# Kernel tuning notes

Measured on AMD Instinct MI355X. Metric: run time of the kernel, lower is better.

Reference implementation:

```python
import jax, jax.numpy as jnp
import numpy as np

N_NODES = 10000
N_EDGES = 320000
DIM = 256
NUM_HEADS = 8
HEAD_DIM = DIM // NUM_HEADS


def setup_inputs() -> dict:
    key = jax.random.key(0)
    ks = jax.random.split(key, 8)
    s = 1.0 / np.sqrt(DIM)
    x = jax.random.normal(ks[0], (N_NODES, DIM), dtype=jnp.float32)
    src = jax.random.randint(ks[1], (N_EDGES,), 0, N_NODES, dtype=jnp.int32)
    dst = jax.random.randint(ks[2], (N_EDGES,), 0, N_NODES, dtype=jnp.int32)
    Wq = jax.random.normal(ks[3], (DIM, DIM), dtype=jnp.float32) * s
    Wk = jax.random.normal(ks[4], (DIM, DIM), dtype=jnp.float32) * s
    Wv = jax.random.normal(ks[5], (DIM, DIM), dtype=jnp.float32) * s
    Wo = jax.random.normal(ks[6], (DIM, DIM), dtype=jnp.float32) * s
    z = jnp.zeros((DIM,), dtype=jnp.float32)
    return {"x": x, "src": src, "dst": dst,
            "Wq": Wq, "bq": z, "Wk": Wk, "bk": z,
            "Wv": Wv, "bv": z, "Wo": Wo, "bo": z}


def reference(x, src, dst, Wq, bq, Wk, bk, Wv, bv, Wo, bo):
    N = x.shape[0]
    # nn.Linear: y = x @ W.T + b
    q = (x @ Wq.T + bq).reshape(N, NUM_HEADS, HEAD_DIM)
    k = (x @ Wk.T + bk).reshape(N, NUM_HEADS, HEAD_DIM)
    v = (x @ Wv.T + bv).reshape(N, NUM_HEADS, HEAD_DIM)
    # u_dot_v: dot(q[src], k[dst]) per head -> [E, H]
    score = jnp.einsum('ehd,ehd->eh', q[src], k[dst]) / np.sqrt(HEAD_DIM).astype(np.float32)
    # Faithful to source: F.softmax(dim=1) on [E, H, 1] -> softmax over HEADS axis
    attn = jax.nn.softmax(score, axis=1)  # [E, H]
    # u_mul_e then sum-reduce onto destination nodes
    m = v[src] * attn[:, :, None]  # [E, H, HEAD_DIM]
    h = jax.ops.segment_sum(m, dst, num_segments=N).reshape(N, DIM)
    out = h @ Wo.T + bo
    # dropout p=0.0 -> identity
    return out
```

## Files before the change

### kernel.cpp

```cpp
#include <hip/hip_runtime.h>
#include <stdint.h>

#define N_NODES 10000
#define N_EDGES 320000
#define DIM 256
#define NRANGE 4
#define RANGE_DIV 2500
#define PAD_SLOTS 32

typedef _Float16 half8 __attribute__((ext_vector_type(8)));
typedef _Float16 half2t __attribute__((ext_vector_type(2)));
typedef float floatx4 __attribute__((ext_vector_type(4)));

#define QK_SCALE 0.17677669529663687f

typedef __attribute__((address_space(3))) uint32_t lds_u32;
typedef __attribute__((address_space(1))) const uint32_t glob_u32;
__device__ __forceinline__ void load16_lds(const _Float16* g, _Float16* l) {
  __builtin_amdgcn_global_load_lds((glob_u32*)g, (lds_u32*)l, 16, 0, 0);
}

__device__ __forceinline__ half8 cvt8s(const float4 a, const float4 b, float sc) {
  half8 o;
  o[0] = (_Float16)(a.x * sc); o[1] = (_Float16)(a.y * sc);
  o[2] = (_Float16)(a.z * sc); o[3] = (_Float16)(a.w * sc);
  o[4] = (_Float16)(b.x * sc); o[5] = (_Float16)(b.y * sc);
  o[6] = (_Float16)(b.z * sc); o[7] = (_Float16)(b.w * sc);
  return o;
}

__global__ void __launch_bounds__(256) prep_k(
    const float* __restrict__ x, const float* __restrict__ Wq,
    const float* __restrict__ Wk, const float* __restrict__ Wv,
    const float* __restrict__ Wo, const int* __restrict__ src,
    const int* __restrict__ dst,
    _Float16* __restrict__ xh, _Float16* __restrict__ Wcat,
    _Float16* __restrict__ Woh, int* __restrict__ cnt4,
    int* __restrict__ slist4) {
  int b = blockIdx.x;
  int t = threadIdx.x;
  if (b < 1250) {
    int i = b * 256 + t;
    const float4* p = (const float4*)x;
    ((half8*)xh)[i] = cvt8s(p[2 * i], p[2 * i + 1], 1.0f);
  } else if (b < 1378) {
    int bb = b - 1250;
    int w = bb >> 5;
    int i = (bb & 31) * 256 + t;
    const float* in = (w == 0) ? Wq : (w == 1) ? Wv : (w == 2) ? Wk : Wo;
    _Float16* out = (w < 3) ? (Wcat + (size_t)w * 65536) : Woh;
    float sc = (w == 0) ? QK_SCALE : 1.0f;
    const float4* p = (const float4*)in;
    ((half8*)out)[i] = cvt8s(p[2 * i], p[2 * i + 1], sc);
  } else {
    int e = (b - 1378) * 256 + t;
    int s = src[e];
    int r = s / RANGE_DIV;
    int cell = dst[e] * NRANGE + r;
    int pos = atomicAdd(&cnt4[cell], 1);
    if (pos < PAD_SLOTS) slist4[cell * PAD_SLOTS + pos] = s;
  }
}

template <int MODE>
__global__ void __launch_bounds__(256) gemm_tiled(
    const _Float16* __restrict__ A, const _Float16* __restrict__ B,
    const float* __restrict__ b0, const float* __restrict__ b1,
    const float* __restrict__ b2,
    _Float16* __restrict__ qv, _Float16* __restrict__ kh,
    float* __restrict__ outf, int M) {
  __shared__ _Float16 As[16384];
  __shared__ _Float16 Bs[16384];
  int t = threadIdx.x;
  int lane = t & 63;
  int wid = t >> 6;
  int l16 = lane & 15;
  int quad = lane >> 4;
  int wm = wid >> 1, wn = wid & 1;
  int m0 = blockIdx.x * 128;
  int n0 = blockIdx.y * 128;

  floatx4 acc[4][4];
#pragma unroll
  for (int i = 0; i < 4; ++i)
#pragma unroll
    for (int j = 0; j < 4; ++j) acc[i][j] = (floatx4){0.f, 0.f, 0.f, 0.f};

  auto stage = [&](int ks, int buf) {
#pragma unroll
    for (int i = 0; i < 4; ++i) {
      int idx = i * 4 + wid;
      int c = idx >> 1;
      int h = idx & 1;
      int r = h * 64 + lane;
      int ar = m0 + r;
      if (ar >= M) ar = M - 1;
      load16_lds(A + (size_t)ar * 256 + ks * 64 + c * 8,
                 &As[buf * 8192 + (c * 128 + h * 64) * 8]);
      load16_lds(B + (size_t)(n0 + r) * 256 + ks * 64 + c * 8,
                 &Bs[buf * 8192 + (c * 128 + h * 64) * 8]);
    }
  };

  stage(0, 0);
  __syncthreads();

  for (int ks = 0; ks < 4; ++ks) {
    int bsel = ks & 1;
    if (ks < 3) stage(ks + 1, 1 - bsel);
#pragma unroll
    for (int kk = 0; kk < 2; ++kk) {
      int j = kk * 4 + quad;
      half8 af[4], bf[4];
#pragma unroll
      for (int i = 0; i < 4; ++i) {
        af[i] = *(const half8*)&As[bsel * 8192 + (j * 128 + wm * 64 + i * 16 + l16) * 8];
        bf[i] = *(const half8*)&Bs[bsel * 8192 + (j * 128 + wn * 64 + i * 16 + l16) * 8];
      }
#pragma unroll
      for (int mi = 0; mi < 4; ++mi)
#pragma unroll
        for (int ni = 0; ni < 4; ++ni)
          acc[mi][ni] =
              __builtin_amdgcn_mfma_f32_16x16x32_f16(af[mi], bf[ni], acc[mi][ni], 0, 0, 0);
    }
    __syncthreads();
  }

#pragma unroll
  for (int mi = 0; mi < 4; ++mi) {
#pragma unroll
    for (int ni = 0; ni < 4; ++ni) {
      int col = n0 + wn * 64 + ni * 16 + l16;
      float bias;
      if (MODE == 0) {
        bias = (col < 256) ? b0[col] * QK_SCALE
                           : (col < 512) ? b1[col - 256] : b2[col - 512];
      } else {
        bias = b0[col];
      }
#pragma unroll
      for (int r = 0; r < 4; ++r) {
        int row = m0 + wm * 64 + mi * 16 + quad * 4 + r;
        if (row < M) {
          float val = acc[mi][ni][r] + bias;
          if (MODE == 0) {
            if (col < 512)
              qv[(size_t)row * 512 + col] = (_Float16)val;
            else
              kh[(size_t)row * 256 + (col - 512)] = (_Float16)val;
          } else {
            outf[(size_t)row * 256 + col] = val;
          }
        }
      }
    }
  }
}

__global__ void __launch_bounds__(256, 4) aggregate_k(
    const _Float16* __restrict__ qv, const _Float16* __restrict__ kh,
    const int* __restrict__ slist4, const int* __restrict__ cnt4,
    _Float16* __restrict__ hh) {
  int lane = threadIdx.x & 63;
  int n = blockIdx.x * 4 + (threadIdx.x >> 6);
  if (n >= N_NODES) return;
  int h = lane & 7;
  int g = lane >> 3;

  int4 cv = ((const int4*)cnt4)[n];
  int d0 = min(cv.x, PAD_SLOTS), d1 = min(cv.y, PAD_SLOTS);
  int d2 = min(cv.z, PAD_SLOTS), d3 = min(cv.w, PAD_SLOTS);
  int o1 = d0, o2 = o1 + d1, o3 = o2 + d2;
  int T = o3 + d3;
  const int* nb = slist4 + (size_t)n * (NRANGE * PAD_SLOTS);

  int sidA = 0, sidB = 0;
  {
    int i0 = lane;
    int r0 = (i0 >= o1) + (i0 >= o2) + (i0 >= o3);
    int b0r = (r0 == 0) ? 0 : (r0 == 1) ? o1 : (r0 == 2) ? o2 : o3;
    if (i0 < T) sidA = nb[r0 * PAD_SLOTS + (i0 - b0r)];
    if (T > 64) {
      int i1 = lane + 64;
      int r1 = (i1 >= o1) + (i1 >= o2) + (i1 >= o3);
      int b1r = (r1 == 0) ? 0 : (r1 == 1) ? o1 : (r1 == 2) ? o2 : o3;
      if (i1 < T) sidB = nb[r1 * PAD_SLOTS + (i1 - b1r)];
    }
  }

  half8 kc[4];
  const half8* krow = (const half8*)(kh + (size_t)n * DIM + h * 32);
#pragma unroll
  for (int i = 0; i < 4; ++i) kc[i] = krow[i];
  const half2t* k2 = (const half2t*)kc;

  half2t acc[16];
#pragma unroll
  for (int i = 0; i < 16; ++i) acc[i] = (half2t){(_Float16)0.f, (_Float16)0.f};

  int iters = (T + 7) >> 3;
  if (iters > 0) {
    int s0 = __shfl(sidA, g);
    const half8* rr = (const half8*)(qv + (size_t)s0 * 512 + h * 32);
    half8 qc[4];
#pragma unroll
    for (int i = 0; i < 4; ++i) qc[i] = rr[i];
    bool valid = g < T;

#pragma unroll 1
    for (int jj = 0; jj < iters; ++jj) {
      half8 vc[4];
#pragma unroll
      for (int i = 0; i < 4; ++i) vc[i] = rr[32 + i];
      half8 nq[4];
      bool nvalid = false;
      const half8* nrr = rr;
      if (jj + 1 < iters) {
        int nidx = (jj + 1) * 8 + g;
        int ns = (jj + 1 < 8) ? __shfl(sidA, nidx) : __shfl(sidB, nidx - 64);
        nrr = (const half8*)(qv + (size_t)ns * 512 + h * 32);
#pragma unroll
        for (int i = 0; i < 4; ++i) nq[i] = nrr[i];
        nvalid = nidx < T;
      }
      const half2t* q2 = (const half2t*)qc;
      float pa = 0.f, pb = 0.f, pc = 0.f, pd = 0.f;
#pragma unroll
      for (int i = 0; i < 4; ++i) {
#if __has_builtin(__builtin_amdgcn_fdot2)
        pa = __builtin_amdgcn_fdot2(q2[i], k2[i], pa, false);
        pb = __builtin_amdgcn_fdot2(q2[4 + i], k2[4 + i], pb, false);
        pc = __builtin_amdgcn_fdot2(q2[8 + i], k2[8 + i], pc, false);
        pd = __builtin_amdgcn_fdot2(q2[12 + i], k2[12 + i], pd, false);
#else
        pa += (float)q2[i][0] * (float)k2[i][0] + (float)q2[i][1] * (float)k2[i][1];
        pb += (float)q2[4 + i][0] * (float)k2[4 + i][0] + (float)q2[4 + i][1] * (float)k2[4 + i][1];
        pc += (float)q2[8 + i][0] * (float)k2[8 + i][0] + (float)q2[8 + i][1] * (float)k2[8 + i][1];
        pd += (float)q2[12 + i][0] * (float)k2[12 + i][0] + (float)q2[12 + i][1] * (float)k2[12 + i][1];
#endif
      }
      float p = (pa + pb) + (pc + pd);
      float ex = __expf(p);
      float ssum = ex;
      ssum += __shfl_xor(ssum, 1);
      ssum += __shfl_xor(ssum, 2);
      ssum += __shfl_xor(ssum, 4);
      float a = valid ? (ex * __frcp_rn(ssum)) : 0.f;
      _Float16 ah = (_Float16)a;
      half2t ah2 = (half2t){ah, ah};
      const half2t* v2 = (const half2t*)vc;
#pragma unroll
      for (int i = 0; i < 16; ++i) acc[i] += v2[i] * ah2;
#pragma unroll
      for (int i = 0; i < 4; ++i) qc[i] = nq[i];
      rr = nrr;
      valid = nvalid;
    }
  }

#pragma unroll
  for (int i = 0; i < 16; ++i) {
    union { half2t h2; int v; } u;
    u.h2 = acc[i]; u.v = __shfl_xor(u.v, 8);  acc[i] += u.h2;
    u.h2 = acc[i]; u.v = __shfl_xor(u.v, 16); acc[i] += u.h2;
    u.h2 = acc[i]; u.v = __shfl_xor(u.v, 32); acc[i] += u.h2;
  }
  if (g == 0) {
    half8* hrow = (half8*)(hh + (size_t)n * DIM + h * 32);
    const half8* a8 = (const half8*)acc;
#pragma unroll
    for (int i = 0; i < 4; ++i) hrow[i] = a8[i];
  }
}

extern "C" void kernel_launch(void* const* d_in, const int* in_sizes, int n_in,
                              void* d_out, int out_size, void* d_ws, size_t ws_size,
                              hipStream_t stream) {
  const float* x = (const float*)d_in[0];
  const int* src = (const int*)d_in[1];
  const int* dst = (const int*)d_in[2];
  const float* Wq = (const float*)d_in[3];
  const float* bq = (const float*)d_in[4];
  const float* Wk = (const float*)d_in[5];
  const float* bk = (const float*)d_in[6];
  const float* Wv = (const float*)d_in[7];
  const float* bv = (const float*)d_in[8];
  const float* Wo = (const float*)d_in[9];
  const float* bo = (const float*)d_in[10];

  char* p = (char*)d_ws;
  const size_t SZ_NODE_H = (size_t)N_NODES * DIM * sizeof(_Float16);
  _Float16* xh = (_Float16*)p; p += SZ_NODE_H;
  _Float16* qvv = (_Float16*)p; p += 2 * SZ_NODE_H;
  _Float16* kh = (_Float16*)p; p += SZ_NODE_H;
  _Float16* hh = (_Float16*)p; p += SZ_NODE_H;
  _Float16* Wcat = (_Float16*)p; p += (size_t)768 * 256 * sizeof(_Float16);
  _Float16* Woh = (_Float16*)p; p += (size_t)256 * 256 * sizeof(_Float16);
  int* cnt4 = (int*)p; p += (size_t)N_NODES * NRANGE * sizeof(int);
  int* slist4 = (int*)p; p += (size_t)N_NODES * NRANGE * PAD_SLOTS * sizeof(int);

  hipMemsetAsync(cnt4, 0, (size_t)N_NODES * NRANGE * sizeof(int), stream);

  prep_k<<<2628, 256, 0, stream>>>(x, Wq, Wk, Wv, Wo, src, dst, xh, Wcat, Woh,
                                   cnt4, slist4);

  gemm_tiled<0><<<dim3(79, 6), 256, 0, stream>>>(xh, Wcat, bq, bv, bk, qvv, kh,
                                                 nullptr, N_NODES);

  aggregate_k<<<2500, 256, 0, stream>>>(qvv, kh, slist4, cnt4, hh);

  gemm_tiled<1><<<dim3(79, 2), 256, 0, stream>>>(hh, Woh, bo, nullptr, nullptr,
                                                 nullptr, nullptr, (float*)d_out,
                                                 N_NODES);
}
```

Before: 171.2 us.

## Overlap edge bucketing with QKV GEMM and fold counter zeroing into prep

The separate memset of the per-node counters is replaced by zeroing done inside the prep kernel. The edge-scatter step, which buckets source ids per destination and range with atomics, moves out of prep and into extra blocks of the QKV GEMM launch. This lets the atomic scatter run alongside the GEMM tiles and removes one memset call. The GEMM kernel is split into two specialised non-template kernels. The scatter blocks now compete with GEMM blocks for CUs, and each scatter block processes 582 edges in a strided loop.

```diff
diff --git a/kernel.cpp b/kernel.cpp
--- a/kernel.cpp
+++ b/kernel.cpp
@@ -32,11 +32,9 @@
 __global__ void __launch_bounds__(256) prep_k(
     const float* __restrict__ x, const float* __restrict__ Wq,
     const float* __restrict__ Wk, const float* __restrict__ Wv,
-    const float* __restrict__ Wo, const int* __restrict__ src,
-    const int* __restrict__ dst,
+    const float* __restrict__ Wo,
     _Float16* __restrict__ xh, _Float16* __restrict__ Wcat,
-    _Float16* __restrict__ Woh, int* __restrict__ cnt4,
-    int* __restrict__ slist4) {
+    _Float16* __restrict__ Woh, int* __restrict__ cnt4) {
   int b = blockIdx.x;
   int t = threadIdx.x;
   if (b < 1250) {
@@ -53,22 +51,122 @@
     const float4* p = (const float4*)in;
     ((half8*)out)[i] = cvt8s(p[2 * i], p[2 * i + 1], sc);
   } else {
-    int e = (b - 1378) * 256 + t;
-    int s = src[e];
-    int r = s / RANGE_DIV;
-    int cell = dst[e] * NRANGE + r;
-    int pos = atomicAdd(&cnt4[cell], 1);
-    if (pos < PAD_SLOTS) slist4[cell * PAD_SLOTS + pos] = s;
-  }
-}
-
-template <int MODE>
-__global__ void __launch_bounds__(256) gemm_tiled(
+    int idx = (b - 1378) * 256 + t;
+#pragma unroll
+    for (int k = 0; k < 4; ++k) {
+      int j = idx + k * 2560;
+      if (j < 10000) ((int4*)cnt4)[j] = (int4){0, 0, 0, 0};
+    }
+  }
+}
+
+__global__ void __launch_bounds__(256) gemm0_scatter_k(
     const _Float16* __restrict__ A, const _Float16* __restrict__ B,
     const float* __restrict__ b0, const float* __restrict__ b1,
     const float* __restrict__ b2,
     _Float16* __restrict__ qv, _Float16* __restrict__ kh,
-    float* __restrict__ outf, int M) {
+    const int* __restrict__ src, const int* __restrict__ dst,
+    int* __restrict__ cnt4, int* __restrict__ slist4) {
+  __shared__ _Float16 As[16384];
+  __shared__ _Float16 Bs[16384];
+  int u = blockIdx.x;
+  int t = threadIdx.x;
+
+  if (u >= 474) {
+    int e0 = (u - 474) * 582;
+    int e1 = e0 + 582;
+    if (e1 > N_EDGES) e1 = N_EDGES;
+    for (int e = e0 + t; e < e1; e += 256) {
+      int s = src[e];
+      int r = s / RANGE_DIV;
+      int cell = dst[e] * NRANGE + r;
+      int pos = atomicAdd(&cnt4[cell], 1);
+      if (pos < PAD_SLOTS) slist4[cell * PAD_SLOTS + pos] = s;
+    }
+    return;
+  }
+
+  int bx = u % 79, by = u / 79;
+  int lane = t & 63;
+  int wid = t >> 6;
+  int l16 = lane & 15;
+  int quad = lane >> 4;
+  int wm = wid >> 1, wn = wid & 1;
+  int m0 = bx * 128;
+  int n0 = by * 128;
+
+  floatx4 acc[4][4];
+#pragma unroll
+  for (int i = 0; i < 4; ++i)
+#pragma unroll
+    for (int j = 0; j < 4; ++j) acc[i][j] = (floatx4){0.f, 0.f, 0.f, 0.f};
+
+  auto stage = [&](int ks, int buf) {
+#pragma unroll
+    for (int i = 0; i < 4; ++i) {
+      int idx = i * 4 + wid;
+      int c = idx >> 1;
+      int h = idx & 1;
+      int r = h * 64 + lane;
+      int ar = m0 + r;
+      if (ar >= N_NODES) ar = N_NODES - 1;
+      load16_lds(A + (size_t)ar * 256 + ks * 64 + c * 8,
+                 &As[buf * 8192 + (c * 128 + h * 64) * 8]);
+      load16_lds(B + (size_t)(n0 + r) * 256 + ks * 64 + c * 8,
+                 &Bs[buf * 8192 + (c * 128 + h * 64) * 8]);
+    }
+  };
+
+  stage(0, 0);
+  __syncthreads();
+
+  for (int ks = 0; ks < 4; ++ks) {
+    int bsel = ks & 1;
+    if (ks < 3) stage(ks + 1, 1 - bsel);
+#pragma unroll
+    for (int kk = 0; kk < 2; ++kk) {
+      int j = kk * 4 + quad;
+      half8 af[4], bf[4];
+#pragma unroll
+      for (int i = 0; i < 4; ++i) {
+        af[i] = *(const half8*)&As[bsel * 8192 + (j * 128 + wm * 64 + i * 16 + l16) * 8];
+        bf[i] = *(const half8*)&Bs[bsel * 8192 + (j * 128 + wn * 64 + i * 16 + l16) * 8];
+      }
+#pragma unroll
+      for (int mi = 0; mi < 4; ++mi)
+#pragma unroll
+        for (int ni = 0; ni < 4; ++ni)
+          acc[mi][ni] =
+              __builtin_amdgcn_mfma_f32_16x16x32_f16(af[mi], bf[ni], acc[mi][ni], 0, 0, 0);
+    }
+    __syncthreads();
+  }
+
+#pragma unroll
+  for (int mi = 0; mi < 4; ++mi) {
+#pragma unroll
+    for (int ni = 0; ni < 4; ++ni) {
+      int col = n0 + wn * 64 + ni * 16 + l16;
+      float bias = (col < 256) ? b0[col] * QK_SCALE
+                               : (col < 512) ? b1[col - 256] : b2[col - 512];
+#pragma unroll
+      for (int r = 0; r < 4; ++r) {
+        int row = m0 + wm * 64 + mi * 16 + quad * 4 + r;
+        if (row < N_NODES) {
+          float val = acc[mi][ni][r] + bias;
+          if (col < 512)
+            qv[(size_t)row * 512 + col] = (_Float16)val;
+          else
+            kh[(size_t)row * 256 + (col - 512)] = (_Float16)val;
+        }
+      }
+    }
+  }
+}
+
+__global__ void __launch_bounds__(256) gemm1_k(
+    const _Float16* __restrict__ A, const _Float16* __restrict__ B,
+    const float* __restrict__ b0, float* __restrict__ outf) {
   __shared__ _Float16 As[16384];
   __shared__ _Float16 Bs[16384];
   int t = threadIdx.x;
@@ -94,7 +192,7 @@
       int h = idx & 1;
       int r = h * 64 + lane;
       int ar = m0 + r;
-      if (ar >= M) ar = M - 1;
+      if (ar >= N_NODES) ar = N_NODES - 1;
       load16_lds(A + (size_t)ar * 256 + ks * 64 + c * 8,
                  &As[buf * 8192 + (c * 128 + h * 64) * 8]);
       load16_lds(B + (size_t)(n0 + r) * 256 + ks * 64 + c * 8,
@@ -132,27 +230,12 @@
 #pragma unroll
     for (int ni = 0; ni < 4; ++ni) {
       int col = n0 + wn * 64 + ni * 16 + l16;
-      float bias;
-      if (MODE == 0) {
-        bias = (col < 256) ? b0[col] * QK_SCALE
-                           : (col < 512) ? b1[col - 256] : b2[col - 512];
-      } else {
-        bias = b0[col];
-      }
+      float bias = b0[col];
 #pragma unroll
       for (int r = 0; r < 4; ++r) {
         int row = m0 + wm * 64 + mi * 16 + quad * 4 + r;
-        if (row < M) {
-          float val = acc[mi][ni][r] + bias;
-          if (MODE == 0) {
-            if (col < 512)
-              qv[(size_t)row * 512 + col] = (_Float16)val;
-            else
-              kh[(size_t)row * 256 + (col - 512)] = (_Float16)val;
-          } else {
-            outf[(size_t)row * 256 + col] = val;
-          }
-        }
+        if (row < N_NODES)
+          outf[(size_t)row * 256 + col] = acc[mi][ni][r] + bias;
       }
     }
   }
@@ -300,17 +383,12 @@
   int* cnt4 = (int*)p; p += (size_t)N_NODES * NRANGE * sizeof(int);
   int* slist4 = (int*)p; p += (size_t)N_NODES * NRANGE * PAD_SLOTS * sizeof(int);
 
-  hipMemsetAsync(cnt4, 0, (size_t)N_NODES * NRANGE * sizeof(int), stream);
-
-  prep_k<<<2628, 256, 0, stream>>>(x, Wq, Wk, Wv, Wo, src, dst, xh, Wcat, Woh,
-                                   cnt4, slist4);
-
-  gemm_tiled<0><<<dim3(79, 6), 256, 0, stream>>>(xh, Wcat, bq, bv, bk, qvv, kh,
-                                                 nullptr, N_NODES);
+  prep_k<<<1388, 256, 0, stream>>>(x, Wq, Wk, Wv, Wo, xh, Wcat, Woh, cnt4);
+
+  gemm0_scatter_k<<<1024, 256, 0, stream>>>(xh, Wcat, bq, bv, bk, qvv, kh,
+                                            src, dst, cnt4, slist4);
 
   aggregate_k<<<2500, 256, 0, stream>>>(qvv, kh, slist4, cnt4, hh);
 
-  gemm_tiled<1><<<dim3(79, 2), 256, 0, stream>>>(hh, Woh, bo, nullptr, nullptr,
-                                                 nullptr, nullptr, (float*)d_out,
-                                                 N_NODES);
-}
+  gemm1_k<<<dim3(79, 2), 256, 0, stream>>>(hh, Woh, bo, (float*)d_out);
+}
```

Measured after the change: 165.8 us. 3.2% less time.

## Overlap edge scatter with QKV GEMM and halve GEMM K-tile LDS

Applied to the files above, without the earlier changes.

The edge bucketing scatter moves out of the prep kernel and into extra blocks of the QKV GEMM launch, so the atomics run alongside the matrix multiply. The counter memset is replaced by zeroing inside prep_k. The GEMM K-step shrinks from 64 to 32, which halves shared memory per block (allowing more resident blocks) but doubles the loop iterations and barriers. The cost is contention between the two kinds of blocks and more synchronisation per tile.

```diff
diff --git a/kernel.cpp b/kernel.cpp
--- a/kernel.cpp
+++ b/kernel.cpp
@@ -32,11 +32,9 @@
 __global__ void __launch_bounds__(256) prep_k(
     const float* __restrict__ x, const float* __restrict__ Wq,
     const float* __restrict__ Wk, const float* __restrict__ Wv,
-    const float* __restrict__ Wo, const int* __restrict__ src,
-    const int* __restrict__ dst,
+    const float* __restrict__ Wo,
     _Float16* __restrict__ xh, _Float16* __restrict__ Wcat,
-    _Float16* __restrict__ Woh, int* __restrict__ cnt4,
-    int* __restrict__ slist4) {
+    _Float16* __restrict__ Woh, int* __restrict__ cnt4) {
   int b = blockIdx.x;
   int t = threadIdx.x;
   if (b < 1250) {
@@ -53,32 +51,25 @@
     const float4* p = (const float4*)in;
     ((half8*)out)[i] = cvt8s(p[2 * i], p[2 * i + 1], sc);
   } else {
-    int e = (b - 1378) * 256 + t;
-    int s = src[e];
-    int r = s / RANGE_DIV;
-    int cell = dst[e] * NRANGE + r;
-    int pos = atomicAdd(&cnt4[cell], 1);
-    if (pos < PAD_SLOTS) slist4[cell * PAD_SLOTS + pos] = s;
-  }
-}
-
-template <int MODE>
-__global__ void __launch_bounds__(256) gemm_tiled(
+    int idx = (b - 1378) * 256 + t;
+#pragma unroll
+    for (int k = 0; k < 4; ++k) {
+      int j = idx + k * 2560;
+      if (j < 10000) ((int4*)cnt4)[j] = (int4){0, 0, 0, 0};
+    }
+  }
+}
+
+template <typename STORE>
+__device__ __forceinline__ void gemm_tile32(
+    _Float16* As, _Float16* Bs,
     const _Float16* __restrict__ A, const _Float16* __restrict__ B,
-    const float* __restrict__ b0, const float* __restrict__ b1,
-    const float* __restrict__ b2,
-    _Float16* __restrict__ qv, _Float16* __restrict__ kh,
-    float* __restrict__ outf, int M) {
-  __shared__ _Float16 As[16384];
-  __shared__ _Float16 Bs[16384];
-  int t = threadIdx.x;
+    int m0, int n0, int t, STORE&& store_fn) {
   int lane = t & 63;
   int wid = t >> 6;
   int l16 = lane & 15;
   int quad = lane >> 4;
   int wm = wid >> 1, wn = wid & 1;
-  int m0 = blockIdx.x * 128;
-  int n0 = blockIdx.y * 128;
 
   floatx4 acc[4][4];
 #pragma unroll
@@ -88,42 +79,38 @@
 
   auto stage = [&](int ks, int buf) {
 #pragma unroll
-    for (int i = 0; i < 4; ++i) {
+    for (int i = 0; i < 2; ++i) {
       int idx = i * 4 + wid;
       int c = idx >> 1;
-      int h = idx & 1;
-      int r = h * 64 + lane;
+      int hh2 = idx & 1;
+      int r = hh2 * 64 + lane;
       int ar = m0 + r;
-      if (ar >= M) ar = M - 1;
-      load16_lds(A + (size_t)ar * 256 + ks * 64 + c * 8,
-                 &As[buf * 8192 + (c * 128 + h * 64) * 8]);
-      load16_lds(B + (size_t)(n0 + r) * 256 + ks * 64 + c * 8,
-                 &Bs[buf * 8192 + (c * 128 + h * 64) * 8]);
+      if (ar >= N_NODES) ar = N_NODES - 1;
+      load16_lds(A + (size_t)ar * 256 + ks * 32 + c * 8,
+                 &As[buf * 4096 + (c * 128 + hh2 * 64) * 8]);
+      load16_lds(B + (size_t)(n0 + r) * 256 + ks * 32 + c * 8,
+                 &Bs[buf * 4096 + (c * 128 + hh2 * 64) * 8]);
     }
   };
 
   stage(0, 0);
   __syncthreads();
 
-  for (int ks = 0; ks < 4; ++ks) {
+  for (int ks = 0; ks < 8; ++ks) {
     int bsel = ks & 1;
-    if (ks < 3) stage(ks + 1, 1 - bsel);
-#pragma unroll
-    for (int kk = 0; kk < 2; ++kk) {
-      int j = kk * 4 + quad;
-      half8 af[4], bf[4];
-#pragma unroll
-      for (int i = 0; i < 4; ++i) {
-        af[i] = *(const half8*)&As[bsel * 8192 + (j * 128 + wm * 64 + i * 16 + l16) * 8];
-        bf[i] = *(const half8*)&Bs[bsel * 8192 + (j * 128 + wn * 64 + i * 16 + l16) * 8];
-      }
-#pragma unroll
-      for (int mi = 0; mi < 4; ++mi)
-#pragma unroll
-        for (int ni = 0; ni < 4; ++ni)
-          acc[mi][ni] =
-              __builtin_amdgcn_mfma_f32_16x16x32_f16(af[mi], bf[ni], acc[mi][ni], 0, 0, 0);
-    }
+    if (ks < 7) stage(ks + 1, 1 - bsel);
+    half8 af[4], bf[4];
+#pragma unroll
+    for (int i = 0; i < 4; ++i) {
+      af[i] = *(const half8*)&As[bsel * 4096 + (quad * 128 + wm * 64 + i * 16 + l16) * 8];
+      bf[i] = *(const half8*)&Bs[bsel * 4096 + (quad * 128 + wn * 64 + i * 16 + l16) * 8];
+    }
+#pragma unroll
+    for (int mi = 0; mi < 4; ++mi)
+#pragma unroll
+      for (int ni = 0; ni < 4; ++ni)
+        acc[mi][ni] =
+            __builtin_amdgcn_mfma_f32_16x16x32_f16(af[mi], bf[ni], acc[mi][ni], 0, 0, 0);
     __syncthreads();
   }
 
@@ -132,30 +119,64 @@
 #pragma unroll
     for (int ni = 0; ni < 4; ++ni) {
       int col = n0 + wn * 64 + ni * 16 + l16;
-      float bias;
-      if (MODE == 0) {
-        bias = (col < 256) ? b0[col] * QK_SCALE
-                           : (col < 512) ? b1[col - 256] : b2[col - 512];
-      } else {
-        bias = b0[col];
-      }
 #pragma unroll
       for (int r = 0; r < 4; ++r) {
         int row = m0 + wm * 64 + mi * 16 + quad * 4 + r;
-        if (row < M) {
-          float val = acc[mi][ni][r] + bias;
-          if (MODE == 0) {
-            if (col < 512)
-              qv[(size_t)row * 512 + col] = (_Float16)val;
-            else
-              kh[(size_t)row * 256 + (col - 512)] = (_Float16)val;
-          } else {
-            outf[(size_t)row * 256 + col] = val;
-          }
-        }
+        if (row < N_NODES) store_fn(row, col, acc[mi][ni][r]);
       }
     }
   }
+}
+
+__global__ void __launch_bounds__(256) gemm0_scatter_k(
+    const _Float16* __restrict__ A, const _Float16* __restrict__ B,
+    const float* __restrict__ b0, const float* __restrict__ b1,
+    const float* __restrict__ b2,
+    _Float16* __restrict__ qv, _Float16* __restrict__ kh,
+    const int* __restrict__ src, const int* __restrict__ dst,
+    int* __restrict__ cnt4, int* __restrict__ slist4) {
+  __shared__ _Float16 As[8192];
+  __shared__ _Float16 Bs[8192];
+  int u = blockIdx.x;
+  int t = threadIdx.x;
+
+  if (u >= 474) {
+    int e0 = (u - 474) * 582;
+    int e1 = e0 + 582;
+    if (e1 > N_EDGES) e1 = N_EDGES;
+    for (int e = e0 + t; e < e1; e += 256) {
+      int s = src[e];
+      int r = s / RANGE_DIV;
+      int cell = dst[e] * NRANGE + r;
+      int pos = atomicAdd(&cnt4[cell], 1);
+      if (pos < PAD_SLOTS) slist4[cell * PAD_SLOTS + pos] = s;
+    }
+    return;
+  }
+
+  int bx = u % 79, by = u / 79;
+  gemm_tile32(As, Bs, A, B, bx * 128, by * 128, t,
+              [&](int row, int col, float v) {
+                float bias = (col < 256) ? b0[col] * QK_SCALE
+                                         : (col < 512) ? b1[col - 256] : b2[col - 512];
+                float val = v + bias;
+                if (col < 512)
+                  qv[(size_t)row * 512 + col] = (_Float16)val;
+                else
+                  kh[(size_t)row * 256 + (col - 512)] = (_Float16)val;
+              });
+}
+
+__global__ void __launch_bounds__(256) gemm1_k(
+    const _Float16* __restrict__ A, const _Float16* __restrict__ B,
+    const float* __restrict__ b0, float* __restrict__ outf) {
+  __shared__ _Float16 As[8192];
+  __shared__ _Float16 Bs[8192];
+  int t = threadIdx.x;
+  gemm_tile32(As, Bs, A, B, blockIdx.x * 128, blockIdx.y * 128, t,
+              [&](int row, int col, float v) {
+                outf[(size_t)row * 256 + col] = v + b0[col];
+              });
 }
 
 __global__ void __launch_bounds__(256, 4) aggregate_k(
@@ -300,17 +321,12 @@
   int* cnt4 = (int*)p; p += (size_t)N_NODES * NRANGE * sizeof(int);
   int* slist4 = (int*)p; p += (size_t)N_NODES * NRANGE * PAD_SLOTS * sizeof(int);
 
-  hipMemsetAsync(cnt4, 0, (size_t)N_NODES * NRANGE * sizeof(int), stream);
-
-  prep_k<<<2628, 256, 0, stream>>>(x, Wq, Wk, Wv, Wo, src, dst, xh, Wcat, Woh,
-                                   cnt4, slist4);
-
-  gemm_tiled<0><<<dim3(79, 6), 256, 0, stream>>>(xh, Wcat, bq, bv, bk, qvv, kh,
-                                                 nullptr, N_NODES);
+  prep_k<<<1388, 256, 0, stream>>>(x, Wq, Wk, Wv, Wo, xh, Wcat, Woh, cnt4);
+
+  gemm0_scatter_k<<<1024, 256, 0, stream>>>(xh, Wcat, bq, bv, bk, qvv, kh,
+                                            src, dst, cnt4, slist4);
 
   aggregate_k<<<2500, 256, 0, stream>>>(qvv, kh, slist4, cnt4, hh);
 
-  gemm_tiled<1><<<dim3(79, 2), 256, 0, stream>>>(hh, Woh, bo, nullptr, nullptr,
-                                                 nullptr, nullptr, (float*)d_out,
-                                                 N_NODES);
-}
+  gemm1_k<<<dim3(79, 2), 256, 0, stream>>>(hh, Woh, bo, (float*)d_out);
+}
```

New measurement: 166.7 us. -2.7%, faster.
